# Performance work log

Measured on AMD Instinct MI355X. Metric: run time of the kernel, lower is better.

The kernel has to match this reference:

```python
import jax, jax.numpy as jnp
import numpy as np

# ---- static config (mirrors YOLOH_Expand cfg) ----
H, W = 200, 200            # feature map size
A = 9                      # num_anchors
C = 80                     # num_classes
M = H * W * A              # total anchors
K = 1000                   # topk NMS candidates
STRIDE = 16
CTR_CLAMP = 32.0
CONF_THRESH = 0.05
NMS_THRESH = 0.6
SCALE_CLAMP = float(np.log(1000.0 / 16))  # DEFAULT_SCALE_CLAMP
ANCHOR_SIZES = np.array([[32,32],[64,64],[128,128],[32,64],[64,32],
                         [64,128],[128,64],[128,256],[256,128]], dtype=np.float32)


def make_anchors():
    # generate_anchors: meshgrid (+0.5)*stride centers, tiled anchor sizes -> (M,4) cxcywh
    ys, xs = np.meshgrid(np.arange(H), np.arange(W), indexing='ij')
    xy = (np.stack([xs, ys], -1).reshape(-1, 2).astype(np.float32) + 0.5) * STRIDE  # (HW,2)
    xy = np.repeat(xy[:, None, :], A, axis=1)                                       # (HW,A,2)
    wh = np.broadcast_to(ANCHOR_SIZES[None], (H * W, A, 2)).astype(np.float32)
    return jnp.asarray(np.concatenate([xy, wh], -1).reshape(-1, 4))


def setup_inputs() -> dict:
    key = jax.random.key(0)
    k1, k2 = jax.random.split(key)
    return {
        'cls_pred': jax.random.normal(k1, (1, M, C), jnp.float32) - 2.0,  # logits, mostly low conf
        'reg_pred': jax.random.normal(k2, (1, M, 4), jnp.float32) * 0.5,
        'anchor_boxes': make_anchors(),
    }


def decode_boxes(anchors, reg):
    # decode_boxes: clamped center offset + clamped log-scale wh -> x1y1x2y2
    ctr_off = jnp.clip(reg[..., :2] * anchors[..., 2:], -CTR_CLAMP, CTR_CLAMP)
    ctr_xy = anchors[..., :2] + ctr_off
    dwdh = jnp.minimum(reg[..., 2:], SCALE_CLAMP)
    wh = anchors[..., 2:] * jnp.exp(dwdh)
    return jnp.concatenate([ctr_xy - 0.5 * wh, ctr_xy + 0.5 * wh], axis=-1)


def pairwise_iou(b):
    # exact math of YOLOH_Expand.nms
    x1, y1, x2, y2 = b[:, 0], b[:, 1], b[:, 2], b[:, 3]
    areas = (x2 - x1) * (y2 - y1)
    xx1 = jnp.maximum(x1[:, None], x1[None, :])
    yy1 = jnp.maximum(y1[:, None], y1[None, :])
    xx2 = jnp.minimum(x2[:, None], x2[None, :])
    yy2 = jnp.minimum(y2[:, None], y2[None, :])
    w = jnp.maximum(1e-28, xx2 - xx1)
    h = jnp.maximum(1e-28, yy2 - yy1)
    inter = w * h
    return inter / (areas[:, None] + areas[None, :] - inter + 1e-14)


def greedy_nms_keep(iou, cls_ids, valid):
    # per-class greedy NMS over score-sorted candidates: box i is suppressed if
    # any kept higher-score box j of the same class has IoU > thresh.
    same = cls_ids[:, None] == cls_ids[None, :]           # (K,K)
    idx = jnp.arange(K)

    def body(keep, i):
        prior = idx < i
        sup = jnp.any(keep & prior & same[i] & (iou[i] > NMS_THRESH))
        keep = keep.at[i].set((~sup) & valid[i])
        return keep, None

    keep0 = jnp.zeros((K,), dtype=bool)
    keep, _ = jax.lax.scan(body, keep0, idx)
    return keep


def reference(cls_pred, reg_pred, anchor_boxes):
    scores = jax.nn.sigmoid(cls_pred[0])                  # (M,C)
    boxes = decode_boxes(anchor_boxes, reg_pred[0])       # (M,4)
    # postprocess: per-anchor best class + confidence threshold
    cls_inds = jnp.argmax(scores, axis=1)                 # (M,)
    sc = jnp.max(scores, axis=1)                          # (M,)
    valid = sc >= CONF_THRESH
    # fixed-size top-k candidate set (invalid ranked last)
    _, top_i = jax.lax.top_k(jnp.where(valid, sc, -1.0), K)
    b = boxes[top_i]                                      # (K,4)
    s = sc[top_i]                                         # (K,)
    c = cls_inds[top_i]                                   # (K,)
    v = valid[top_i]                                      # (K,)
    iou = pairwise_iou(b)                                 # (K,K)
    keep = greedy_nms_keep(iou, c, v)                     # (K,) bool
    return b, s * keep.astype(s.dtype), c.astype(jnp.int32), keep
```

## Files before the change

### kernel.cpp

```cpp
#include <hip/hip_runtime.h>
#include <math.h>

typedef unsigned long long u64;
typedef unsigned int u32;

#define M_ANCH 360000
#define NCLS 80
#define KTOP 1000
#define CAP 8192
#define NBINS 65536
#define RREP 64
#define CONF_THRESH 0.05f
#define NMS_THRESH 0.6f
#define CTR_CLAMP 32.0f
#define SCALE_CLAMP 4.1351665567423560f

#define AS1 __attribute__((address_space(1)))
#define AS3 __attribute__((address_space(3)))

#define HIST_OFF   0u
#define HIST_BYTES (RREP * NBINS * 2u)
#define CNT_OFF    (HIST_OFF + HIST_BYTES)
#define B_OFF      (CNT_OFF + 4u)
#define VW_OFF     (B_OFF + 4u + 8u)
#define DONE_OFF   (VW_OFF + 128u)
#define ZERO_END   (DONE_OFF + 16u)
#define MERGED_OFF ((ZERO_END + 15u) & ~15u)
#define BLKSUM_OFF (MERGED_OFF + NBINS * 4u)
#define CAND_OFF   (BLKSUM_OFF + 256u)
#define SC_OFF     (CAND_OFF + CAP * 8u)
#define CLS_OFF    (SC_OFF + M_ANCH * 4u)
#define SSC_OFF    (CLS_OFF + M_ANCH * 4u)
#define SCLS_OFF   (SSC_OFF + KTOP * 4u)
#define SUP_OFF    ((SCLS_OFF + KTOP * 4u + 15u) & ~15u)

#define NTILES 5625
#define SCORE_GRID 1024
#define SUPNMS_GRID 125

__device__ __forceinline__ u32 fkey(float f) {
    u32 u = __float_as_uint(f);
    return (u & 0x80000000u) ? ~u : (u | 0x80000000u);
}
__device__ __forceinline__ float unfkey(u32 u) {
    u32 f = (u & 0x80000000u) ? (u & 0x7FFFFFFFu) : ~u;
    return __uint_as_float(f);
}

__global__ __launch_bounds__(256) void k_score(const float* __restrict__ cls_pred,
                                               float* __restrict__ sc_all,
                                               int* __restrict__ cls_all,
                                               u32* __restrict__ hist) {
    __shared__ float4 stage[2][1280];
    const int t = threadIdx.x;
    const int w = t >> 6;
    const int l = t & 63;
    const int q = l >> 2;
    const int p = l & 3;

    int tile = blockIdx.x;
    {
        const float4* gp = (const float4*)cls_pred + (size_t)tile * 1280;
#pragma unroll
        for (int k = 0; k < 5; k++) {
            int f = t + 256 * k;
            __builtin_amdgcn_global_load_lds((AS1 void*)(gp + f),
                                             (AS3 void*)(&stage[0][f]), 16, 0, 0);
        }
    }
    int cur = 0;
    for (; tile < NTILES; tile += SCORE_GRID) {
        int next = tile + SCORE_GRID;
        if (next < NTILES) {
            const float4* gp = (const float4*)cls_pred + (size_t)next * 1280;
#pragma unroll
            for (int k = 0; k < 5; k++) {
                int f = t + 256 * k;
                __builtin_amdgcn_global_load_lds((AS1 void*)(gp + f),
                                                 (AS3 void*)(&stage[cur ^ 1][f]), 16, 0, 0);
            }
            if (tile == (int)blockIdx.x) {
                asm volatile("s_waitcnt vmcnt(5)" ::: "memory");
            } else {
                asm volatile("s_waitcnt vmcnt(8)" ::: "memory");
            }
        } else {
            asm volatile("s_waitcnt vmcnt(0)" ::: "memory");
        }
        __builtin_amdgcn_s_barrier();
        __builtin_amdgcn_sched_barrier(0);

        const float4* av = &stage[cur][(16 * w + q) * 20];
        float mv = -1e30f; int mc = 0;
#pragma unroll
        for (int i = 0; i < 5; i++) {
            int k = 5 * p + ((i + q) % 5);
            float4 v = av[k];
            float lm_ = v.x; int lc_ = 4 * k;
            if (v.y > lm_) { lm_ = v.y; lc_ = 4 * k + 1; }
            if (v.z > lm_) { lm_ = v.z; lc_ = 4 * k + 2; }
            if (v.w > lm_) { lm_ = v.w; lc_ = 4 * k + 3; }
            if (lm_ > mv || (lm_ == mv && lc_ < mc)) { mv = lm_; mc = lc_; }
        }
        u64 key = ((u64)fkey(mv) << 32) | (u64)(~(u32)mc);
        u64 o = __shfl_xor(key, 1); if (o > key) key = o;
        o = __shfl_xor(key, 2);     if (o > key) key = o;
        if (p == 0) {
            int a = tile * 64 + 16 * w + q;
            float lv = unfkey((u32)(key >> 32));
            float sc = 1.0f / (1.0f + expf(-lv));
            sc_all[a] = sc;
            cls_all[a] = (int)(~(u32)key);
            float msk = (sc >= CONF_THRESH) ? sc : -1.0f;
            u32 rep = ((u32)tile * 7u + (u32)w) & (RREP - 1);
            u32 bin = fkey(msk) >> 16;
            atomicAdd(&hist[(rep << 15) + (bin >> 1)], 1u << ((bin & 1) << 4));
        }
        __builtin_amdgcn_s_barrier();
        __builtin_amdgcn_sched_barrier(0);
        cur ^= 1;
    }
}

__global__ __launch_bounds__(1024) void k_hsum_boundary(const u32* __restrict__ hist,
                                                        u32* __restrict__ merged,
                                                        u32* __restrict__ blksum,
                                                        u32* __restrict__ done,
                                                        u32* __restrict__ outB) {
    __shared__ u32 red[1024];
    __shared__ u32 bs[64];
    __shared__ u32 sj, sA;
    __shared__ int sflag;
    int t = threadIdx.x;
    int b = blockIdx.x * 1024 + t;
    int word = b >> 1;
    int sh = (b & 1) << 4;
    u32 s = 0;
#pragma unroll 8
    for (int r = 0; r < RREP; r++) s += (hist[(r << 15) + word] >> sh) & 0xFFFFu;
    merged[b] = s;
    red[t] = s;
    __syncthreads();
    for (int off = 512; off > 0; off >>= 1) {
        if (t < off) red[t] += red[t + off];
        __syncthreads();
    }
    if (t == 0) blksum[blockIdx.x] = red[0];
    __syncthreads();
    if (t == 0) {
        __threadfence();
        sflag = (atomicAdd(done, 1u) == 63u) ? 1 : 0;
    }
    __syncthreads();
    if (!sflag) return;
    if (t == 0) __threadfence();
    __syncthreads();

    if (t < 64) bs[t] = blksum[t];
    __syncthreads();
    if (t == 0) {
        u32 cum = 0; u32 j = 0; u32 Aj = 0;
        for (int i = 63; i >= 0; i--) {
            if (cum + bs[i] >= KTOP) { j = (u32)i; Aj = cum; break; }
            cum += bs[i];
        }
        sj = j; sA = Aj;
    }
    __syncthreads();
    u32 j = sj, Aj = sA;
    u32 h = merged[j * 1024 + t];
    red[t] = h;
    __syncthreads();
    u32 v = h;
    for (int off = 1; off < 1024; off <<= 1) {
        u32 add = (t + off < 1024) ? red[t + off] : 0u;
        __syncthreads();
        v += add;
        red[t] = v;
        __syncthreads();
    }
    u32 above = (t == 1023) ? 0u : red[t + 1];
    if (Aj + above < KTOP && Aj + above + h >= KTOP) outB[0] = j * 1024 + t;
}

__global__ __launch_bounds__(1024) void k_compact_select(const float* __restrict__ sc_all,
                                                         const int* __restrict__ cls_all,
                                                         const u32* __restrict__ pB,
                                                         const float* __restrict__ reg_pred,
                                                         const float* __restrict__ anchors,
                                                         u32* __restrict__ counter,
                                                         u64* __restrict__ cand,
                                                         u32* __restrict__ done,
                                                         float* __restrict__ out,
                                                         float* __restrict__ sel_sc,
                                                         int* __restrict__ sel_cls,
                                                         u64* __restrict__ valid_words) {
    __shared__ u64 keys[CAP];
    __shared__ int sflag;
    int t = threadIdx.x;
    int i4 = blockIdx.x * 1024 + t;
    if (i4 < M_ANCH / 4) {
        u32 B = *pB;
        float4 s4 = ((const float4*)sc_all)[i4];
        float se[4] = { s4.x, s4.y, s4.z, s4.w };
#pragma unroll
        for (int e = 0; e < 4; e++) {
            float m = (se[e] >= CONF_THRESH) ? se[e] : -1.0f;
            u32 u = fkey(m);
            if ((u >> 16) >= B) {
                u32 pos = atomicAdd(counter, 1u);
                if (pos < CAP)
                    cand[pos] = ((u64)u << 32) | (u64)(0xFFFFFFFFu - (u32)(4 * i4 + e));
            }
        }
    }
    __syncthreads();
    if (t == 0) {
        __threadfence();
        sflag = (atomicAdd(done, 1u) == gridDim.x - 1) ? 1 : 0;
    }
    __syncthreads();
    if (!sflag) return;
    if (t == 0) __threadfence();
    __syncthreads();

    u32 n = *counter;
    if (n > CAP) n = CAP;
    u32 P = 1024;
    while (P < n) P <<= 1;
    for (u32 i = t; i < P; i += 1024) keys[i] = (i < n) ? cand[i] : 0ull;
    for (u32 k = 2; k <= P; k <<= 1) {
        for (u32 j = k >> 1; j > 0; j >>= 1) {
            __syncthreads();
            for (u32 i = t; i < P; i += 1024) {
                u32 ixj = i ^ j;
                if (ixj > i) {
                    u64 a = keys[i], bb = keys[ixj];
                    bool desc = ((i & k) == 0);
                    if (desc ? (a < bb) : (a > bb)) { keys[i] = bb; keys[ixj] = a; }
                }
            }
        }
    }
    __syncthreads();
    if (t < KTOP) {
        u64 key = keys[t];
        u32 idx = 0xFFFFFFFFu - (u32)(key & 0xFFFFFFFFull);
        if (idx >= M_ANCH) idx = 0;
        float s = sc_all[idx];
        int cl = cls_all[idx];
        float4 a = ((const float4*)anchors)[idx];
        float4 r = ((const float4*)reg_pred)[idx];
        float ox = fminf(fmaxf(r.x * a.z, -CTR_CLAMP), CTR_CLAMP);
        float oy = fminf(fmaxf(r.y * a.w, -CTR_CLAMP), CTR_CLAMP);
        float cx = a.x + ox, cy = a.y + oy;
        float ww = a.z * expf(fminf(r.z, SCALE_CLAMP));
        float hh = a.w * expf(fminf(r.w, SCALE_CLAMP));
        float4 box;
        box.x = cx - 0.5f * ww;
        box.y = cy - 0.5f * hh;
        box.z = cx + 0.5f * ww;
        box.w = cy + 0.5f * hh;
        ((float4*)out)[t] = box;
        out[5 * KTOP + t] = (float)cl;
        sel_sc[t] = s;
        sel_cls[t] = cl;
        if (s >= CONF_THRESH) atomicOr(&valid_words[t >> 6], 1ull << (t & 63));
    }
}

__global__ __launch_bounds__(1024) void k_supmat_nms(const float* __restrict__ outb,
                                                     const int* __restrict__ sel_cls,
                                                     u64* __restrict__ sup,
                                                     u32* __restrict__ done,
                                                     const u64* __restrict__ valid_words,
                                                     const float* __restrict__ sel_sc,
                                                     float* __restrict__ out) {
    __shared__ u64 keepA[16];
    __shared__ int sflag;
    int t = threadIdx.x;
    int wid = t >> 6;
    int lane = t & 63;
    int base = blockIdx.x * 128 + wid * 8;
#pragma unroll
    for (int k = 0; k < 8; k++) {
        int g = base + k;
        int i = g >> 4;
        int w = g & 15;
        if (w * 64 > i) {
            if (lane == 0) sup[g] = 0ull;
            continue;
        }
        int j = w * 64 + lane;
        int jc = (j < KTOP) ? j : (KTOP - 1);
        float4 bi = ((const float4*)outb)[i];
        float4 bj = ((const float4*)outb)[jc];
        int ci = sel_cls[i], cj = sel_cls[jc];
        float ai = (bi.z - bi.x) * (bi.w - bi.y);
        float aj = (bj.z - bj.x) * (bj.w - bj.y);
        float xx1 = fmaxf(bi.x, bj.x), yy1 = fmaxf(bi.y, bj.y);
        float xx2 = fminf(bi.z, bj.z), yy2 = fminf(bi.w, bj.w);
        float iw = fmaxf(1e-28f, xx2 - xx1), ih = fmaxf(1e-28f, yy2 - yy1);
        float inter = iw * ih;
        float iou = inter / (ai + aj - inter + 1e-14f);
        bool pred = (j < i) && (ci == cj) && (iou > NMS_THRESH);
        u64 bal = __ballot((int)pred);
        if (lane == 0) sup[g] = bal;
    }
    __syncthreads();
    if (t == 0) {
        __threadfence();
        sflag = (atomicAdd(done, 1u) == SUPNMS_GRID - 1) ? 1 : 0;
    }
    __syncthreads();
    if (!sflag) return;
    if (t == 0) __threadfence();
    __syncthreads();

    int row = wid * 64 + lane;
    int rowc = (row < KTOP) ? row : (KTOP - 1);
    const ulonglong2* rp = (const ulonglong2*)(sup + (size_t)rowc * 16);
    ulonglong2 q0 = rp[0], q1 = rp[1], q2 = rp[2], q3 = rp[3];
    ulonglong2 q4 = rp[4], q5 = rp[5], q6 = rp[6], q7 = rp[7];
    u64 d  = sup[(size_t)rowc * 16 + wid];
    u64 vm = valid_words[wid];

    if (t < 16) keepA[t] = 0ull;
    __syncthreads();

    for (int b = 0; b < 16; b++) {
        if (wid == b) {
            u64 acc = (q0.x & keepA[0])  | (q0.y & keepA[1])
                    | (q1.x & keepA[2])  | (q1.y & keepA[3])
                    | (q2.x & keepA[4])  | (q2.y & keepA[5])
                    | (q3.x & keepA[6])  | (q3.y & keepA[7])
                    | (q4.x & keepA[8])  | (q4.y & keepA[9])
                    | (q5.x & keepA[10]) | (q5.y & keepA[11])
                    | (q6.x & keepA[12]) | (q6.y & keepA[13])
                    | (q7.x & keepA[14]) | (q7.y & keepA[15]);
            u64 premask = __ballot(acc != 0ull);
            u64 eligible = vm & ~premask;

            u32 dlo = (u32)d, dhi = (u32)(d >> 32);
            u64 kb = 0ull;
#pragma unroll
            for (int jj = 0; jj < 64; jj++) {
                u32 djl = __builtin_amdgcn_readlane(dlo, jj);
                u32 djh = __builtin_amdgcn_readlane(dhi, jj);
                u64 dj = ((u64)djh << 32) | (u64)djl;
                bool kj = (((eligible >> jj) & 1ull) != 0ull) && ((dj & kb) == 0ull);
                kb |= ((u64)(kj ? 1u : 0u)) << jj;
            }
            if (lane == 0) keepA[b] = kb;
        }
        __syncthreads();
    }

    if (t < KTOP) {
        int kb = (int)((keepA[t >> 6] >> (t & 63)) & 1ull);
        float s = sel_sc[t];
        out[4 * KTOP + t] = kb ? s : 0.0f;
        out[6 * KTOP + t] = (float)kb;
    }
}

extern "C" void kernel_launch(void* const* d_in, const int* in_sizes, int n_in,
                              void* d_out, int out_size, void* d_ws, size_t ws_size,
                              hipStream_t stream) {
    const float* cls_pred = (const float*)d_in[0];
    const float* reg_pred = (const float*)d_in[1];
    const float* anchors  = (const float*)d_in[2];
    float* out = (float*)d_out;
    char* ws = (char*)d_ws;

    u32* hist     = (u32*)(ws + HIST_OFF);
    u32* counter  = (u32*)(ws + CNT_OFF);
    u32* pB       = (u32*)(ws + B_OFF);
    u64* vwords   = (u64*)(ws + VW_OFF);
    u32* dones    = (u32*)(ws + DONE_OFF);
    u32* merged   = (u32*)(ws + MERGED_OFF);
    u32* blksum   = (u32*)(ws + BLKSUM_OFF);
    u64* cand     = (u64*)(ws + CAND_OFF);
    float* sc_all = (float*)(ws + SC_OFF);
    int* cls_all  = (int*)(ws + CLS_OFF);
    float* sel_sc = (float*)(ws + SSC_OFF);
    int* sel_cls  = (int*)(ws + SCLS_OFF);
    u64* sup      = (u64*)(ws + SUP_OFF);

    hipMemsetAsync(d_ws, 0, ZERO_END, stream);

    k_score<<<SCORE_GRID, 256, 0, stream>>>(cls_pred, sc_all, cls_all, hist);
    k_hsum_boundary<<<NBINS / 1024, 1024, 0, stream>>>(hist, merged, blksum,
                                                       &dones[0], pB);
    int ncs = (M_ANCH / 4 + 1023) / 1024;
    k_compact_select<<<ncs, 1024, 0, stream>>>(sc_all, cls_all, pB, reg_pred,
                                               anchors, counter, cand, &dones[1],
                                               out, sel_sc, sel_cls, vwords);
    k_supmat_nms<<<SUPNMS_GRID, 1024, 0, stream>>>(out, sel_cls, sup, &dones[2],
                                                   vwords, sel_sc, out);
}
```

Baseline: 277.5 us.

## Restructure score kernel into 32-anchor units with 4-stage LDS pipeline and deferred epilogue

The scoring kernel now processes 32-anchor units instead of 64-anchor tiles, keeping three loads in flight through a 4-buffer LDS ring. The per-unit loop is unrolled at compile time per block, and 8 lanes cooperate on each anchor's 80-class argmax. Results are held in registers, and the sigmoid, global stores and histogram atomics are deferred to an epilogue after all loads finish. This aims to hide more memory latency and move atomics and stores off the critical load path, at the cost of more registers and uneven per-block work (11 vs 10 units).

```diff
diff --git a/kernel.cpp b/kernel.cpp
--- a/kernel.cpp
+++ b/kernel.cpp
@@ -34,7 +34,7 @@
 #define SCLS_OFF   (SSC_OFF + KTOP * 4u)
 #define SUP_OFF    ((SCLS_OFF + KTOP * 4u + 15u) & ~15u)
 
-#define NTILES 5625
+#define UNITS 11250
 #define SCORE_GRID 1024
 #define SUPNMS_GRID 125
 
@@ -47,79 +47,140 @@
     return __uint_as_float(f);
 }
 
-__global__ __launch_bounds__(256) void k_score(const float* __restrict__ cls_pred,
-                                               float* __restrict__ sc_all,
-                                               int* __restrict__ cls_all,
-                                               u32* __restrict__ hist) {
-    __shared__ float4 stage[2][1280];
-    const int t = threadIdx.x;
-    const int w = t >> 6;
-    const int l = t & 63;
-    const int q = l >> 2;
-    const int p = l & 3;
-
-    int tile = blockIdx.x;
-    {
-        const float4* gp = (const float4*)cls_pred + (size_t)tile * 1280;
-#pragma unroll
-        for (int k = 0; k < 5; k++) {
-            int f = t + 256 * k;
-            __builtin_amdgcn_global_load_lds((AS1 void*)(gp + f),
-                                             (AS3 void*)(&stage[0][f]), 16, 0, 0);
-        }
-    }
-    int cur = 0;
-    for (; tile < NTILES; tile += SCORE_GRID) {
-        int next = tile + SCORE_GRID;
-        if (next < NTILES) {
-            const float4* gp = (const float4*)cls_pred + (size_t)next * 1280;
-#pragma unroll
-            for (int k = 0; k < 5; k++) {
-                int f = t + 256 * k;
-                __builtin_amdgcn_global_load_lds((AS1 void*)(gp + f),
-                                                 (AS3 void*)(&stage[cur ^ 1][f]), 16, 0, 0);
-            }
-            if (tile == (int)blockIdx.x) {
-                asm volatile("s_waitcnt vmcnt(5)" ::: "memory");
-            } else {
-                asm volatile("s_waitcnt vmcnt(8)" ::: "memory");
-            }
-        } else {
-            asm volatile("s_waitcnt vmcnt(0)" ::: "memory");
-        }
+template<int N>
+__device__ __forceinline__ void vwait() {
+    if constexpr (N == 0) asm volatile("s_waitcnt vmcnt(0)" ::: "memory");
+    else if constexpr (N == 2) asm volatile("s_waitcnt vmcnt(2)" ::: "memory");
+    else if constexpr (N == 3) asm volatile("s_waitcnt vmcnt(3)" ::: "memory");
+    else if constexpr (N == 4) asm volatile("s_waitcnt vmcnt(4)" ::: "memory");
+    else if constexpr (N == 6) asm volatile("s_waitcnt vmcnt(6)" ::: "memory");
+    else if constexpr (N == 9) asm volatile("s_waitcnt vmcnt(9)" ::: "memory");
+}
+
+template<int NTU, int I>
+__device__ __forceinline__ void score_iter(const float* __restrict__ cls_pred,
+                                           float4 (*__restrict__ buf)[640],
+                                           int u0, int t, int al, int r,
+                                           bool lowhalf,
+                                           float (&rlv)[11], u32 (&rcls)[11]) {
+    if constexpr (I < NTU) {
+        if constexpr (I + 3 < NTU) {
+            const float4* gp = (const float4*)cls_pred +
+                               (size_t)(u0 + (I + 3) * SCORE_GRID) * 640;
+            __builtin_amdgcn_global_load_lds((AS1 void*)(gp + t),
+                                             (AS3 void*)(&buf[(I + 3) & 3][t]), 16, 0, 0);
+            __builtin_amdgcn_global_load_lds((AS1 void*)(gp + 256 + t),
+                                             (AS3 void*)(&buf[(I + 3) & 3][256 + t]), 16, 0, 0);
+            if (lowhalf)
+                __builtin_amdgcn_global_load_lds((AS1 void*)(gp + 512 + t),
+                                                 (AS3 void*)(&buf[(I + 3) & 3][512 + t]), 16, 0, 0);
+        }
+        constexpr int MM = ((NTU - 1 - I) < 3) ? (NTU - 1 - I) : 3;
+        if (lowhalf) vwait<3 * MM>(); else vwait<2 * MM>();
         __builtin_amdgcn_s_barrier();
         __builtin_amdgcn_sched_barrier(0);
 
-        const float4* av = &stage[cur][(16 * w + q) * 20];
+        const float4* av = &buf[I & 3][al * 20];
         float mv = -1e30f; int mc = 0;
-#pragma unroll
-        for (int i = 0; i < 5; i++) {
-            int k = 5 * p + ((i + q) % 5);
-            float4 v = av[k];
+        {
+            float4 v = av[r]; int k = r;
             float lm_ = v.x; int lc_ = 4 * k;
             if (v.y > lm_) { lm_ = v.y; lc_ = 4 * k + 1; }
             if (v.z > lm_) { lm_ = v.z; lc_ = 4 * k + 2; }
             if (v.w > lm_) { lm_ = v.w; lc_ = 4 * k + 3; }
             if (lm_ > mv || (lm_ == mv && lc_ < mc)) { mv = lm_; mc = lc_; }
         }
+        {
+            float4 v = av[r + 8]; int k = r + 8;
+            float lm_ = v.x; int lc_ = 4 * k;
+            if (v.y > lm_) { lm_ = v.y; lc_ = 4 * k + 1; }
+            if (v.z > lm_) { lm_ = v.z; lc_ = 4 * k + 2; }
+            if (v.w > lm_) { lm_ = v.w; lc_ = 4 * k + 3; }
+            if (lm_ > mv || (lm_ == mv && lc_ < mc)) { mv = lm_; mc = lc_; }
+        }
+        if (r < 4) {
+            float4 v = av[r + 16]; int k = r + 16;
+            float lm_ = v.x; int lc_ = 4 * k;
+            if (v.y > lm_) { lm_ = v.y; lc_ = 4 * k + 1; }
+            if (v.z > lm_) { lm_ = v.z; lc_ = 4 * k + 2; }
+            if (v.w > lm_) { lm_ = v.w; lc_ = 4 * k + 3; }
+            if (lm_ > mv || (lm_ == mv && lc_ < mc)) { mv = lm_; mc = lc_; }
+        }
         u64 key = ((u64)fkey(mv) << 32) | (u64)(~(u32)mc);
         u64 o = __shfl_xor(key, 1); if (o > key) key = o;
         o = __shfl_xor(key, 2);     if (o > key) key = o;
-        if (p == 0) {
-            int a = tile * 64 + 16 * w + q;
-            float lv = unfkey((u32)(key >> 32));
-            float sc = 1.0f / (1.0f + expf(-lv));
-            sc_all[a] = sc;
-            cls_all[a] = (int)(~(u32)key);
+        o = __shfl_xor(key, 4);     if (o > key) key = o;
+        if (r == 0) { rlv[I] = unfkey((u32)(key >> 32)); rcls[I] = ~(u32)key; }
+
+        __builtin_amdgcn_s_barrier();
+        __builtin_amdgcn_sched_barrier(0);
+
+        score_iter<NTU, I + 1>(cls_pred, buf, u0, t, al, r, lowhalf, rlv, rcls);
+    }
+}
+
+template<int NTU, int I>
+__device__ __forceinline__ void score_epi(float* __restrict__ sc_all,
+                                          int* __restrict__ cls_all,
+                                          u32* __restrict__ hist,
+                                          int u0, int al, int r, int w,
+                                          float (&rlv)[11], u32 (&rcls)[11]) {
+    if constexpr (I < NTU) {
+        if (r == 0) {
+            int gu = u0 + I * SCORE_GRID;
+            int A = gu * 32 + al;
+            float sc = 1.0f / (1.0f + expf(-rlv[I]));
+            sc_all[A] = sc;
+            cls_all[A] = (int)rcls[I];
             float msk = (sc >= CONF_THRESH) ? sc : -1.0f;
-            u32 rep = ((u32)tile * 7u + (u32)w) & (RREP - 1);
+            u32 rep = ((u32)gu * 7u + (u32)w) & (RREP - 1);
             u32 bin = fkey(msk) >> 16;
             atomicAdd(&hist[(rep << 15) + (bin >> 1)], 1u << ((bin & 1) << 4));
         }
-        __builtin_amdgcn_s_barrier();
-        __builtin_amdgcn_sched_barrier(0);
-        cur ^= 1;
-    }
+        score_epi<NTU, I + 1>(sc_all, cls_all, hist, u0, al, r, w, rlv, rcls);
+    }
+}
+
+template<int NTU>
+__device__ __forceinline__ void score_body(const float* __restrict__ cls_pred,
+                                           float* __restrict__ sc_all,
+                                           int* __restrict__ cls_all,
+                                           u32* __restrict__ hist,
+                                           float4 (*__restrict__ buf)[640]) {
+    const int t = threadIdx.x;
+    const int u0 = blockIdx.x;
+    const int w = t >> 6;
+    const int al = t >> 3;
+    const int r = t & 7;
+    const bool lowhalf = (t < 128);
+
+    float rlv[11]; u32 rcls[11];
+
+#pragma unroll
+    for (int j = 0; j < 3; j++) {
+        const float4* gp = (const float4*)cls_pred + (size_t)(u0 + j * SCORE_GRID) * 640;
+        __builtin_amdgcn_global_load_lds((AS1 void*)(gp + t),
+                                         (AS3 void*)(&buf[j][t]), 16, 0, 0);
+        __builtin_amdgcn_global_load_lds((AS1 void*)(gp + 256 + t),
+                                         (AS3 void*)(&buf[j][256 + t]), 16, 0, 0);
+        if (lowhalf)
+            __builtin_amdgcn_global_load_lds((AS1 void*)(gp + 512 + t),
+                                             (AS3 void*)(&buf[j][512 + t]), 16, 0, 0);
+    }
+
+    score_iter<NTU, 0>(cls_pred, buf, u0, t, al, r, lowhalf, rlv, rcls);
+    score_epi<NTU, 0>(sc_all, cls_all, hist, u0, al, r, w, rlv, rcls);
+}
+
+__global__ __launch_bounds__(256) void k_score(const float* __restrict__ cls_pred,
+                                               float* __restrict__ sc_all,
+                                               int* __restrict__ cls_all,
+                                               u32* __restrict__ hist) {
+    __shared__ float4 buf[4][640];
+    if ((int)blockIdx.x < UNITS - 10 * SCORE_GRID)
+        score_body<11>(cls_pred, sc_all, cls_all, hist, buf);
+    else
+        score_body<10>(cls_pred, sc_all, cls_all, hist, buf);
 }
 
 __global__ __launch_bounds__(1024) void k_hsum_boundary(const u32* __restrict__ hist,
```

New measurement: 283.8 us. +2.3%, slower.

## Replace LDS-staged double buffering with direct per-wave global loads in score kernel

Applied to the files above, without the earlier changes.

The score kernel no longer stages tiles of class logits through LDS with async global_load_lds double buffering and block barriers. Each wave now handles 8 anchors per iteration, reading float4 values straight from global memory, with 8 lanes per anchor and one extra shuffle step for the argmax. The grid is doubled to keep enough loads in flight without explicit pipelining. This removes the LDS traffic and barrier stalls but relies on the hardware to hide latency, and the rep hashing for the histogram replicas changes to depend on the anchor index. Loads now alternate between full and partial lane use, since only lanes with r<4 read the third float4.

```diff
diff --git a/kernel.cpp b/kernel.cpp
--- a/kernel.cpp
+++ b/kernel.cpp
@@ -14,9 +14,6 @@
 #define NMS_THRESH 0.6f
 #define CTR_CLAMP 32.0f
 #define SCALE_CLAMP 4.1351665567423560f
-
-#define AS1 __attribute__((address_space(1)))
-#define AS3 __attribute__((address_space(3)))
 
 #define HIST_OFF   0u
 #define HIST_BYTES (RREP * NBINS * 2u)
@@ -34,8 +31,8 @@
 #define SCLS_OFF   (SSC_OFF + KTOP * 4u)
 #define SUP_OFF    ((SCLS_OFF + KTOP * 4u + 15u) & ~15u)
 
-#define NTILES 5625
-#define SCORE_GRID 1024
+#define NCHUNK 45000
+#define SCORE_GRID 2048
 #define SUPNMS_GRID 125
 
 __device__ __forceinline__ u32 fkey(float f) {
@@ -51,74 +48,50 @@
                                                float* __restrict__ sc_all,
                                                int* __restrict__ cls_all,
                                                u32* __restrict__ hist) {
-    __shared__ float4 stage[2][1280];
     const int t = threadIdx.x;
-    const int w = t >> 6;
+    const int wave = (int)blockIdx.x * 4 + (t >> 6);
     const int l = t & 63;
-    const int q = l >> 2;
-    const int p = l & 3;
-
-    int tile = blockIdx.x;
-    {
-        const float4* gp = (const float4*)cls_pred + (size_t)tile * 1280;
-#pragma unroll
-        for (int k = 0; k < 5; k++) {
-            int f = t + 256 * k;
-            __builtin_amdgcn_global_load_lds((AS1 void*)(gp + f),
-                                             (AS3 void*)(&stage[0][f]), 16, 0, 0);
-        }
-    }
-    int cur = 0;
-    for (; tile < NTILES; tile += SCORE_GRID) {
-        int next = tile + SCORE_GRID;
-        if (next < NTILES) {
-            const float4* gp = (const float4*)cls_pred + (size_t)next * 1280;
-#pragma unroll
-            for (int k = 0; k < 5; k++) {
-                int f = t + 256 * k;
-                __builtin_amdgcn_global_load_lds((AS1 void*)(gp + f),
-                                                 (AS3 void*)(&stage[cur ^ 1][f]), 16, 0, 0);
-            }
-            if (tile == (int)blockIdx.x) {
-                asm volatile("s_waitcnt vmcnt(5)" ::: "memory");
-            } else {
-                asm volatile("s_waitcnt vmcnt(8)" ::: "memory");
-            }
-        } else {
-            asm volatile("s_waitcnt vmcnt(0)" ::: "memory");
-        }
-        __builtin_amdgcn_s_barrier();
-        __builtin_amdgcn_sched_barrier(0);
-
-        const float4* av = &stage[cur][(16 * w + q) * 20];
-        float mv = -1e30f; int mc = 0;
-#pragma unroll
-        for (int i = 0; i < 5; i++) {
-            int k = 5 * p + ((i + q) % 5);
-            float4 v = av[k];
-            float lm_ = v.x; int lc_ = 4 * k;
-            if (v.y > lm_) { lm_ = v.y; lc_ = 4 * k + 1; }
-            if (v.z > lm_) { lm_ = v.z; lc_ = 4 * k + 2; }
-            if (v.w > lm_) { lm_ = v.w; lc_ = 4 * k + 3; }
-            if (lm_ > mv || (lm_ == mv && lc_ < mc)) { mv = lm_; mc = lc_; }
+    const int g8 = l >> 3;
+    const int r = l & 7;
+    const int NW = (SCORE_GRID * 256) >> 6;
+
+    for (int chunk = wave; chunk < NCHUNK; chunk += NW) {
+        int anchor = chunk * 8 + g8;
+        const float4* ap = (const float4*)cls_pred + (size_t)anchor * 20;
+        float4 v0 = ap[r];
+        float4 v1 = ap[r + 8];
+        float mv; int mc;
+        mv = v0.x; mc = 4 * r;
+        if (v0.y > mv) { mv = v0.y; mc = 4 * r + 1; }
+        if (v0.z > mv) { mv = v0.z; mc = 4 * r + 2; }
+        if (v0.w > mv) { mv = v0.w; mc = 4 * r + 3; }
+        int k1 = r + 8;
+        if (v1.x > mv) { mv = v1.x; mc = 4 * k1; }
+        if (v1.y > mv) { mv = v1.y; mc = 4 * k1 + 1; }
+        if (v1.z > mv) { mv = v1.z; mc = 4 * k1 + 2; }
+        if (v1.w > mv) { mv = v1.w; mc = 4 * k1 + 3; }
+        if (r < 4) {
+            float4 v2 = ap[r + 16];
+            int k2 = r + 16;
+            if (v2.x > mv) { mv = v2.x; mc = 4 * k2; }
+            if (v2.y > mv) { mv = v2.y; mc = 4 * k2 + 1; }
+            if (v2.z > mv) { mv = v2.z; mc = 4 * k2 + 2; }
+            if (v2.w > mv) { mv = v2.w; mc = 4 * k2 + 3; }
         }
         u64 key = ((u64)fkey(mv) << 32) | (u64)(~(u32)mc);
         u64 o = __shfl_xor(key, 1); if (o > key) key = o;
         o = __shfl_xor(key, 2);     if (o > key) key = o;
-        if (p == 0) {
-            int a = tile * 64 + 16 * w + q;
+        o = __shfl_xor(key, 4);     if (o > key) key = o;
+        if (r == 0) {
             float lv = unfkey((u32)(key >> 32));
             float sc = 1.0f / (1.0f + expf(-lv));
-            sc_all[a] = sc;
-            cls_all[a] = (int)(~(u32)key);
+            sc_all[anchor] = sc;
+            cls_all[anchor] = (int)(~(u32)key);
             float msk = (sc >= CONF_THRESH) ? sc : -1.0f;
-            u32 rep = ((u32)tile * 7u + (u32)w) & (RREP - 1);
+            u32 rep = ((u32)anchor * 7u) & (RREP - 1);
             u32 bin = fkey(msk) >> 16;
             atomicAdd(&hist[(rep << 15) + (bin >> 1)], 1u << ((bin & 1) << 4));
         }
-        __builtin_amdgcn_s_barrier();
-        __builtin_amdgcn_sched_barrier(0);
-        cur ^= 1;
     }
 }
 
```

New measurement: 281.4 us. About the same (+1.4%).
